# Kernel tuning notes

Measured on AMD Instinct MI355X. Metric: run time of the kernel, lower is better.

The kernel has to match this reference:

```python
import jax, jax.numpy as jnp
import numpy as np

B_, S_, E_ = 1, 2048, 2048
NH, P_, N_, G_, K_, CS = 64, 64, 128, 1, 4, 256
INTER = NH * P_            # 4096
CONV_DIM = INTER + 2 * G_ * N_  # 4352
PROJ = INTER + CONV_DIM + NH
EPS = 1e-5


def setup_inputs() -> dict:
    key = jax.random.key(0)
    ks = jax.random.split(key, 6)
    return {
        "input_states": jax.random.normal(ks[0], (B_, S_, E_), dtype=jnp.float32),
        "mask": jnp.ones((B_, 1, S_), dtype=jnp.int32),
        "W_in": jax.random.normal(ks[1], (PROJ, E_), dtype=jnp.float32) * 0.02,
        "conv_w": jax.random.normal(ks[2], (CONV_DIM, K_), dtype=jnp.float32) * 0.2,
        "conv_b": jnp.zeros((CONV_DIM,), dtype=jnp.float32),
        "dt_bias": jnp.ones((NH,), dtype=jnp.float32),
        "A_log": jnp.log(jnp.arange(1, NH + 1, dtype=jnp.float32)),
        "D": jnp.ones((NH,), dtype=jnp.float32),
        "norm_w": jnp.ones((INTER,), dtype=jnp.float32),
        "W_out": jax.random.normal(ks[3], (E_, INTER), dtype=jnp.float32) * 0.02,
    }


def segsum(x):
    # x: [..., L]; out[..., i, j] = sum_{j < k <= i} x[..., k], -inf above diagonal
    L = x.shape[-1]
    i = jnp.arange(L)
    strict = i[:, None] > i[None, :]
    X = jnp.where(strict, x[..., :, None], 0.0)   # [..., L(i), L(j)]
    S = jnp.cumsum(X, axis=-2)
    return jnp.where(i[:, None] >= i[None, :], S, -jnp.inf)


def reference(input_states, mask, W_in, conv_w, conv_b, dt_bias, A_log, D, norm_w, W_out):
    B, S, E = input_states.shape
    # mask has shape[1]==1 -> apply_mask_to_padding_states is a no-op
    proj = input_states @ W_in.T                      # [B,S,PROJ]
    gate = proj[..., :INTER]
    h_BC = proj[..., INTER:INTER + CONV_DIM]
    dt = proj[..., INTER + CONV_DIM:]                 # [B,S,NH]

    # causal depthwise conv1d (padding=K-1, truncated to seq_len)
    xpad = jnp.pad(h_BC, ((0, 0), (K_ - 1, 0), (0, 0)))
    conv = conv_b
    for i in range(K_):
        conv = conv + xpad[:, i:i + S, :] * conv_w[:, i]
    h_BC = jax.nn.silu(conv)

    hidden = h_BC[..., :INTER]
    Bm = h_BC[..., INTER:INTER + G_ * N_]
    Cm = h_BC[..., INTER + G_ * N_:]

    A = -jnp.exp(A_log)                               # [NH]
    dt = jnp.clip(jax.nn.softplus(dt + dt_bias), 0.0) # [B,S,NH]

    Hs = hidden.reshape(B, S, NH, P_).astype(jnp.float32)
    Bm = jnp.tile(Bm.reshape(B, S, G_, N_).astype(jnp.float32), (1, 1, NH // G_, 1))
    Cm = jnp.tile(Cm.reshape(B, S, G_, N_).astype(jnp.float32), (1, 1, NH // G_, 1))

    D_resid = D[None, None, :, None] * Hs             # pad=0 since S % CS == 0
    Hdt = Hs * dt[..., None]
    At = A * dt                                       # [B,S,NH]

    C_ = S // CS
    Hc = Hdt.reshape(B, C_, CS, NH, P_)
    Ac = At.reshape(B, C_, CS, NH)
    Bc = Bm.reshape(B, C_, CS, NH, N_)
    Cc = Cm.reshape(B, C_, CS, NH, N_)

    Ap = jnp.transpose(Ac, (0, 3, 1, 2))              # [B,H,C,L]
    A_cum = jnp.cumsum(Ap, axis=-1)                   # [B,H,C,L]
    L_tri = jnp.exp(segsum(Ap))                       # [B,H,C,L,L]

    # diagonal (intra-chunk) output
    Gm = jnp.einsum('bclhn,bcshn->bclsh', Cc, Bc)
    M = Gm * jnp.transpose(L_tri, (0, 2, 3, 4, 1))    # [B,C,L,S,H]
    Yd = jnp.einsum('bclsh,bcshp->bclhp', M, Hc)

    # per-chunk states (note: source uses same-chunk states, no inter-chunk scan)
    decay = jnp.exp(A_cum[..., -1:] - A_cum)          # [B,H,C,L]
    Bd = Bc * jnp.transpose(decay, (0, 2, 3, 1))[..., None]
    states = jnp.einsum('bclhn,bclhp->bchpn', Bd, Hc) # [B,C,H,P,N]

    Sd = jnp.transpose(jnp.exp(A_cum), (0, 2, 3, 1))  # [B,C,L,H]
    Yoff = jnp.einsum('bclhn,bchpn->bclhp', Cc, states) * Sd[..., None]

    y = (Yd + Yoff).reshape(B, S, NH, P_) + D_resid
    y = y.reshape(B, S, INTER)

    # gated RMSNorm (fp32)
    yf = y.astype(jnp.float32) * jax.nn.silu(gate.astype(jnp.float32))
    var = jnp.mean(yf * yf, axis=-1, keepdims=True)
    yn = norm_w * (yf * jax.lax.rsqrt(var + EPS))

    return yn @ W_out.T
```

## Files before the change

### kernel.cpp

```cpp
#include <hip/hip_runtime.h>
#include <math.h>

#define S_LEN   2048
#define E_DIM   2048
#define NH      64
#define P_DIM   64
#define N_DIM   128
#define CS      256
#define NCHUNK  8
#define INTER   4096
#define CONVD   4352
#define PROJ    8512
#define GEMM1N  8448
#define EPS     1e-5f

#define OFF_PROJBF 0ull
#define OFF_HBC    8650752ull
#define OFF_DTG    13107200ull
#define OFF_DTPART 13238272ull
#define OFF_GM     17432576ull
#define OFF_YV     17956864ull
#define OFF_R      26345472ull
#define OFF_WOUT   37093376ull

typedef __bf16 bf16x8 __attribute__((ext_vector_type(8)));
typedef float  f32x4  __attribute__((ext_vector_type(4)));
typedef float  f32x16 __attribute__((ext_vector_type(16)));

__device__ __forceinline__ float bf2f(unsigned short u) {
    union { unsigned int i; float f; } v; v.i = ((unsigned int)u) << 16; return v.f;
}
__device__ __forceinline__ unsigned short f2bf(float f) {
    union { float f; unsigned int i; } v; v.f = f;
    unsigned int r = v.i + 0x7FFFu + ((v.i >> 16) & 1u);
    return (unsigned short)(r >> 16);
}
__device__ __forceinline__ void gl_lds16(const void* g, void* l) {
    __builtin_amdgcn_global_load_lds(
        (const __attribute__((address_space(1))) void*)g,
        (__attribute__((address_space(3))) void*)l, 16, 0, 0);
}

__global__ __launch_bounds__(256) void cast3_kernel(
    const float* __restrict__ X, const float* __restrict__ Win,
    const float* __restrict__ Wout, unsigned short* __restrict__ Xbf,
    unsigned short* __restrict__ Winbf, unsigned short* __restrict__ Woutbf)
{
    const int blk = blockIdx.x;
    const float* src; unsigned short* dst; size_t off;
    if (blk < 2048)       { src = X;    dst = Xbf;    off = (size_t)blk * 2048; }
    else if (blk < 10496) { src = Win;  dst = Winbf;  off = (size_t)(blk - 2048) * 2048; }
    else                  { src = Wout; dst = Woutbf; off = (size_t)(blk - 10496) * 2048; }
    size_t i = off + (size_t)threadIdx.x * 8;
    float4 a = *(const float4*)(src + i);
    float4 b = *(const float4*)(src + i + 4);
    uint4 o;
    o.x = (unsigned int)f2bf(a.x) | ((unsigned int)f2bf(a.y) << 16);
    o.y = (unsigned int)f2bf(a.z) | ((unsigned int)f2bf(a.w) << 16);
    o.z = (unsigned int)f2bf(b.x) | ((unsigned int)f2bf(b.y) << 16);
    o.w = (unsigned int)f2bf(b.z) | ((unsigned int)f2bf(b.w) << 16);
    *(uint4*)(dst + i) = o;
}

#define WAITV(n) asm volatile("s_waitcnt vmcnt(" #n ")" ::: "memory")
#define BARR()   asm volatile("s_barrier" ::: "memory")

__global__ __launch_bounds__(512, 2) void gemm256_8ph(
    const unsigned short* __restrict__ A, int lda, long long sA,
    const unsigned short* __restrict__ B, int ldb, long long sB,
    float* __restrict__ Cf, unsigned short* __restrict__ Cb, int ldc,
    long long sC, int K, int mswap)
{
    __shared__ unsigned short sm[65536];
    A += (long long)blockIdx.z * sA;
    B += (long long)blockIdx.z * sB;
    const int t    = threadIdx.x;
    const int m0   = (mswap ? blockIdx.x : blockIdx.y) * 256;
    const int n0   = (mswap ? blockIdx.y : blockIdx.x) * 256;
    const int lane = t & 63;
    const int w    = t >> 6;
    const int wm   = ((w >> 2) & 1) * 64;
    const int wn   = (w & 3) * 32;
    const int l15  = lane & 15;
    const int l4   = lane >> 4;
    const int NT   = K >> 6;

    const int sr = t >> 3, sl = t & 7;

    auto STAGE = [&](int T, int h, int isB) {
        const unsigned short* G = isB ? B : A;
        const int ld   = isB ? ldb : lda;
        const int base = (isB ? n0 : m0) + h * 128;
        unsigned short* dst =
            &sm[(T & 1) * 32768 + isB * 16384 + h * 8192 + t * 8];
#pragma unroll
        for (int j = 0; j < 2; j++) {
            const int r   = sr + 64 * j;
            const int gch = sl ^ ((r ^ (r >> 3)) & 7);
            gl_lds16(G + (size_t)(base + r) * ld + T * 64 + gch * 8,
                     dst + j * 4096);
        }
    };

    int aoff[4], asw[4], boff[2], bsw[2];
#pragma unroll
    for (int mi = 0; mi < 4; mi++) {
        int r = wm + mi * 16 + l15;
        aoff[mi] = r * 64; asw[mi] = (r ^ (r >> 3)) & 7;
    }
#pragma unroll
    for (int ni = 0; ni < 2; ni++) {
        int r = wn + ni * 16 + l15;
        boff[ni] = r * 64; bsw[ni] = (r ^ (r >> 3)) & 7;
    }

    bf16x8 aF[4][2], bF[2][2][2];
    f32x4  acc[2][2][4][2];
#pragma unroll
    for (int qm = 0; qm < 2; qm++)
#pragma unroll
        for (int qn = 0; qn < 2; qn++)
#pragma unroll
            for (int mi = 0; mi < 4; mi++)
#pragma unroll
                for (int ni = 0; ni < 2; ni++)
                    acc[qm][qn][mi][ni] = (f32x4){0.f, 0.f, 0.f, 0.f};

#define LOAD_A(qm) do { \
    const unsigned short* p_ = &sm[cb + (qm) * 8192]; \
    _Pragma("unroll") for (int mi = 0; mi < 4; mi++) \
    _Pragma("unroll") for (int ks = 0; ks < 2; ks++) \
        aF[mi][ks] = *(const bf16x8*)&p_[aoff[mi] + \
            (((ks * 4 + l4) ^ asw[mi]) << 3)]; \
} while (0)
#define LOAD_B(qn) do { \
    const unsigned short* p_ = &sm[cb + 16384 + (qn) * 8192]; \
    _Pragma("unroll") for (int ni = 0; ni < 2; ni++) \
    _Pragma("unroll") for (int ks = 0; ks < 2; ks++) \
        bF[qn][ni][ks] = *(const bf16x8*)&p_[boff[ni] + \
            (((ks * 4 + l4) ^ bsw[ni]) << 3)]; \
} while (0)
#define MMA(qm, qn) do { \
    __builtin_amdgcn_s_setprio(1); \
    _Pragma("unroll") for (int ks = 0; ks < 2; ks++) \
    _Pragma("unroll") for (int mi = 0; mi < 4; mi++) \
    _Pragma("unroll") for (int ni = 0; ni < 2; ni++) \
        acc[qm][qn][mi][ni] = __builtin_amdgcn_mfma_f32_16x16x32_bf16( \
            aF[mi][ks], bF[qn][ni][ks], acc[qm][qn][mi][ni], 0, 0, 0); \
    __builtin_amdgcn_s_setprio(0); \
} while (0)

    STAGE(0, 0, 0);
    STAGE(0, 1, 1);
    STAGE(0, 0, 1);
    STAGE(0, 1, 0);
    STAGE(1, 0, 0);
    STAGE(1, 1, 1);
    WAITV(0);
    BARR();

    for (int tt = 0; tt < NT; tt++) {
        const int cb = (tt & 1) * 32768;
        if (tt + 1 < NT) { WAITV(6); } else { WAITV(2); }
        LOAD_A(0); LOAD_B(0);
        if (tt + 1 < NT) STAGE(tt + 1, 0, 1);
        BARR();
        MMA(0, 0);
        BARR();
        LOAD_B(1);
        if (tt + 1 < NT) STAGE(tt + 1, 1, 0);
        BARR();
        MMA(0, 1);
        BARR();
        if (tt + 1 < NT) { WAITV(6); } else { WAITV(0); }
        LOAD_A(1);
        if (tt + 2 < NT) STAGE(tt + 2, 0, 0);
        BARR();
        MMA(1, 1);
        BARR();
        if (tt + 2 < NT) STAGE(tt + 2, 1, 1);
        BARR();
        MMA(1, 0);
        BARR();
    }

#undef LOAD_A
#undef LOAD_B
#undef MMA

    if (Cb) {
#pragma unroll
        for (int qm = 0; qm < 2; qm++)
#pragma unroll
        for (int qn = 0; qn < 2; qn++)
#pragma unroll
        for (int mi = 0; mi < 4; mi++)
#pragma unroll
        for (int ni = 0; ni < 2; ni++) {
            const int rb = m0 + qm * 128 + wm + mi * 16 + l4 * 4;
            const int cc = n0 + qn * 128 + wn + ni * 16 + l15;
#pragma unroll
            for (int rr = 0; rr < 4; rr++)
                Cb[(size_t)(rb + rr) * ldc + cc] = f2bf(acc[qm][qn][mi][ni][rr]);
        }
    } else {
        float* Cz = Cf + (long long)blockIdx.z * sC;
#pragma unroll
        for (int qm = 0; qm < 2; qm++)
#pragma unroll
        for (int qn = 0; qn < 2; qn++)
#pragma unroll
        for (int mi = 0; mi < 4; mi++)
#pragma unroll
        for (int ni = 0; ni < 2; ni++) {
            const int rb = m0 + qm * 128 + wm + mi * 16 + l4 * 4;
            const int cc = n0 + qn * 128 + wn + ni * 16 + l15;
#pragma unroll
            for (int rr = 0; rr < 4; rr++)
                Cz[(size_t)(rb + rr) * ldc + cc] = acc[qm][qn][mi][ni][rr];
        }
    }
}

__global__ __launch_bounds__(256) void gemm_bt_mfma(
    const unsigned short* __restrict__ A, int lda, long long sA,
    const unsigned short* __restrict__ B, int ldb, long long sB,
    float* __restrict__ Cf, unsigned short* __restrict__ Cb, int ldc,
    long long sC, int K, int mswap)
{
    __shared__ unsigned short As[128 * 64];
    __shared__ unsigned short Bs[128 * 64];
    A += (long long)blockIdx.z * sA;
    B += (long long)blockIdx.z * sB;
    const int t     = threadIdx.x;
    const int m0    = (mswap ? blockIdx.x : blockIdx.y) * 128;
    const int n0    = (mswap ? blockIdx.y : blockIdx.x) * 128;
    const int w     = t >> 6;
    const int lane  = t & 63;
    const int col   = lane & 31;
    const int khalf = lane >> 5;
    const int wm    = (w & 1) * 64;
    const int wn    = (w >> 1) * 64;

    const int srow  = t >> 3;
    const int sslot = t & 7;
    const unsigned short* Agp[4];
    const unsigned short* Bgp[4];
#pragma unroll
    for (int i = 0; i < 4; i++) {
        const int r   = srow + 32 * i;
        const int gch = sslot ^ ((r ^ (r >> 3)) & 7);
        Agp[i] = A + (size_t)(m0 + r) * lda + gch * 8;
        Bgp[i] = B + (size_t)(n0 + r) * ldb + gch * 8;
    }
    unsigned short* Asl = &As[t * 8];
    unsigned short* Bsl = &Bs[t * 8];

    int aOff[2], aXor[2], bOff[2], bXor[2];
#pragma unroll
    for (int i = 0; i < 2; i++) {
        const int ra = wm + i * 32 + col;
        aOff[i] = ra * 64; aXor[i] = (ra ^ (ra >> 3)) & 7;
        const int rb = wn + i * 32 + col;
        bOff[i] = rb * 64; bXor[i] = (rb ^ (rb >> 3)) & 7;
    }

    f32x16 acc[2][2];
#pragma unroll
    for (int mi = 0; mi < 2; mi++)
#pragma unroll
        for (int ni = 0; ni < 2; ni++)
#pragma unroll
            for (int e = 0; e < 16; e++) acc[mi][ni][e] = 0.f;

    for (int k0 = 0; k0 < K; k0 += 64) {
        __syncthreads();
#pragma unroll
        for (int i = 0; i < 4; i++) {
            gl_lds16(Agp[i] + k0, Asl + i * 2048);
            gl_lds16(Bgp[i] + k0, Bsl + i * 2048);
        }
        __syncthreads();
#pragma unroll
        for (int ks = 0; ks < 4; ks++) {
            const int ch = ks * 2 + khalf;
            bf16x8 af[2], bfr[2];
#pragma unroll
            for (int i = 0; i < 2; i++) {
                af[i]  = *(const bf16x8*)&As[aOff[i] + ((ch ^ aXor[i]) * 8)];
                bfr[i] = *(const bf16x8*)&Bs[bOff[i] + ((ch ^ bXor[i]) * 8)];
            }
#pragma unroll
            for (int mi = 0; mi < 2; mi++)
#pragma unroll
                for (int ni = 0; ni < 2; ni++)
                    acc[mi][ni] = __builtin_amdgcn_mfma_f32_32x32x16_bf16(
                        af[mi], bfr[ni], acc[mi][ni], 0, 0, 0);
        }
    }

    if (Cb) {
#pragma unroll
        for (int mi = 0; mi < 2; mi++)
#pragma unroll
            for (int ni = 0; ni < 2; ni++) {
                const int rbase = m0 + wm + mi * 32 + 4 * khalf;
                const int cc    = n0 + wn + ni * 32 + col;
#pragma unroll
                for (int g = 0; g < 4; g++)
#pragma unroll
                    for (int rr = 0; rr < 4; rr++)
                        Cb[(size_t)(rbase + 8 * g + rr) * ldc + cc] =
                            f2bf(acc[mi][ni][4 * g + rr]);
            }
    } else {
        float* Cz = Cf + (long long)blockIdx.z * sC;
#pragma unroll
        for (int mi = 0; mi < 2; mi++)
#pragma unroll
            for (int ni = 0; ni < 2; ni++) {
                const int rbase = m0 + wm + mi * 32 + 4 * khalf;
                const int cc    = n0 + wn + ni * 32 + col;
#pragma unroll
                for (int g = 0; g < 4; g++)
#pragma unroll
                    for (int rr = 0; rr < 4; rr++)
                        Cz[(size_t)(rbase + 8 * g + rr) * ldc + cc] =
                            acc[mi][ni][4 * g + rr];
            }
    }
}

__global__ __launch_bounds__(256) void addf4_kernel(
    const float* __restrict__ p, float* __restrict__ o)
{
    size_t i = ((size_t)blockIdx.x * 256 + threadIdx.x) * 4;
    float4 a = *(const float4*)(p + i);
    float4 b = *(const float4*)(p + i + 4194304);
    float4 c = *(const float4*)(p + i + 8388608);
    float4 d = *(const float4*)(p + i + 12582912);
    float4 r = make_float4(a.x + b.x + c.x + d.x, a.y + b.y + c.y + d.y,
                           a.z + b.z + c.z + d.z, a.w + b.w + c.w + d.w);
    *(float4*)(o + i) = r;
}

__global__ __launch_bounds__(256) void gemm_nt(
    const float* __restrict__ A, int lda, long long sA,
    const float* __restrict__ B, int ldb, long long sB,
    float* __restrict__ C, int ldc, long long sC, int K)
{
    A += (long long)blockIdx.z * sA;
    B += (long long)blockIdx.z * sB;
    C += (long long)blockIdx.z * sC;
    const int t  = threadIdx.x;
    const int m0 = blockIdx.y * 128;
    const int n0 = blockIdx.x * 64;
    __shared__ float As[16][132];
    __shared__ float Bs[16][68];
    const int tx = t & 15;
    const int ty = t >> 4;

    const int arow = t & 127;
    const int akh  = (t >> 7) * 8;
    const float* Aload = A + (size_t)(m0 + arow) * (size_t)lda + akh;
    const int brow = t & 63;
    const int bk4  = (t >> 6) * 4;
    const float* Bload = B + (size_t)(n0 + brow) * (size_t)ldb + bk4;

    float acc[8][4];
#pragma unroll
    for (int i = 0; i < 8; i++)
#pragma unroll
        for (int j = 0; j < 4; j++) acc[i][j] = 0.f;

    for (int k0 = 0; k0 < K; k0 += 16) {
        __syncthreads();
        float4 a0 = *(const float4*)(Aload + k0);
        float4 a1 = *(const float4*)(Aload + k0 + 4);
        float4 b0 = *(const float4*)(Bload + k0);
        As[akh + 0][arow] = a0.x; As[akh + 1][arow] = a0.y;
        As[akh + 2][arow] = a0.z; As[akh + 3][arow] = a0.w;
        As[akh + 4][arow] = a1.x; As[akh + 5][arow] = a1.y;
        As[akh + 6][arow] = a1.z; As[akh + 7][arow] = a1.w;
        Bs[bk4 + 0][brow] = b0.x; Bs[bk4 + 1][brow] = b0.y;
        Bs[bk4 + 2][brow] = b0.z; Bs[bk4 + 3][brow] = b0.w;
        __syncthreads();
#pragma unroll
        for (int k = 0; k < 16; k++) {
            float4 a4 = *(const float4*)(&As[k][ty * 8]);
            float4 a5 = *(const float4*)(&As[k][ty * 8 + 4]);
            float4 b4 = *(const float4*)(&Bs[k][tx * 4]);
            float am[8] = {a4.x, a4.y, a4.z, a4.w, a5.x, a5.y, a5.z, a5.w};
            float bn[4] = {b4.x, b4.y, b4.z, b4.w};
#pragma unroll
            for (int i = 0; i < 8; i++)
#pragma unroll
                for (int j = 0; j < 4; j++) acc[i][j] += am[i] * bn[j];
        }
    }
#pragma unroll
    for (int i = 0; i < 8; i++) {
        float4 o = make_float4(acc[i][0], acc[i][1], acc[i][2], acc[i][3]);
        *(float4*)(C + (size_t)(m0 + ty * 8 + i) * (size_t)ldc + n0 + tx * 4) = o;
    }
}

__global__ __launch_bounds__(256) void dt_reduce_kernel(
    const float* __restrict__ part, const float* __restrict__ dt_bias,
    float* __restrict__ dtg)
{
    const int i = blockIdx.x * 256 + threadIdx.x;
    float x = dt_bias[i & 63];
#pragma unroll
    for (int z = 0; z < 32; z++) x += part[(size_t)z * 131072 + i];
    dtg[i] = (x > 20.f) ? x : log1pf(__expf(x));
}

__global__ __launch_bounds__(256) void conv_silu8_kernel(
    const unsigned short* __restrict__ projbf, const float* __restrict__ conv_w,
    const float* __restrict__ conv_b, unsigned short* __restrict__ out)
{
    const int c  = blockIdx.x * 256 + threadIdx.x;
    const int s0 = blockIdx.y * 8;
    const float4 w = *(const float4*)(conv_w + (size_t)c * 4);
    const float b = conv_b[c];
    const size_t base = 4096 + (size_t)c;
    float v[11];
#pragma unroll
    for (int m = 0; m < 11; m++) {
        int s = s0 - 3 + m;
        v[m] = (s >= 0) ? bf2f(projbf[(size_t)s * GEMM1N + base]) : 0.f;
    }
#pragma unroll
    for (int j = 0; j < 8; j++) {
        float acc = b + v[j] * w.x + v[j + 1] * w.y + v[j + 2] * w.z + v[j + 3] * w.w;
        float sig = 1.f / (1.f + __expf(-acc));
        out[(size_t)(s0 + j) * CONVD + c] = f2bf(acc * sig);
    }
}

__global__ __launch_bounds__(256, 2) void ssm_mfma_kernel(
    const unsigned short* __restrict__ hBC, const float* __restrict__ dtg,
    const float* __restrict__ Gm, const float* __restrict__ A_log,
    const float* __restrict__ Dp, float* __restrict__ y)
{
    const int h    = blockIdx.x;
    const int c    = blockIdx.y;
    const int t    = threadIdx.x;
    const int wid  = t >> 6;
    const int lane = t & 63;
    const int lo   = lane & 15;
    const int q    = lane >> 4;

    __shared__ float sAcum[CS], sdt[CS], sD[CS], sEs[CS], sDecay[CS], sScl[CS];
    __shared__ float sWaveSum[4];
    __shared__ unsigned short sHdtT[64 * 264];
    __shared__ unsigned short sStT[64 * 136];
    __shared__ unsigned short sBufB[128 * 72];

    const float A = -__expf(A_log[h]);
    const int row0 = c * CS;
    const unsigned short* hid = hBC + (size_t)row0 * CONVD + h * P_DIM;
    const unsigned short* Bp  = hBC + (size_t)row0 * CONVD + INTER;
    const unsigned short* Cp  = hBC + (size_t)row0 * CONVD + INTER + N_DIM;
    const float* gm = Gm + (size_t)c * CS * CS;

    float dtv = dtg[(size_t)(row0 + t) * NH + h];
    float v = A * dtv;
    for (int off = 1; off < 64; off <<= 1) {
        float u = __shfl_up(v, off, 64);
        if (lane >= off) v += u;
    }
    if (lane == 63) sWaveSum[wid] = v;
    __syncthreads();
    float pre = 0.f;
    for (int i = 0; i < 4; i++) if (i < wid) pre += sWaveSum[i];
    v += pre;
    sAcum[t] = v;
    sdt[t] = dtv;
    __syncthreads();
    const float AcumEnd = sAcum[CS - 1];
    {
        float ac   = sAcum[t];
        float apre = (t < 64) ? 0.f : sAcum[(t & ~63) - 1];
        sD[t]     = __expf(ac - apre);
        sEs[t]    = __expf(sAcum[t | 63] - ac);
        sDecay[t] = __expf(AcumEnd - ac);
        sScl[t]   = __expf(ac);
    }

    unsigned short* stgu = sStT;
    for (int lt = 0; lt < 4; lt++) {
        __syncthreads();
        {
            const int c8 = (t & 7) * 8;
#pragma unroll
            for (int j = 0; j < 2; j++) {
                int l = (t >> 3) + 32 * j;
                *(uint4*)&stgu[l * 64 + c8] =
                    *(const uint4*)(hid + (size_t)(lt * 64 + l) * CONVD + c8);
            }
        }
        __syncthreads();
        {
            const int p = t & 63, lq = (t >> 6) * 16;
#pragma unroll
            for (int j = 0; j < 4; j++) {
                ushort4 pk;
                int l0 = lq + j * 4;
                pk.x = f2bf(bf2f(stgu[(l0 + 0) * 64 + p]) * sdt[lt * 64 + l0 + 0]);
                pk.y = f2bf(bf2f(stgu[(l0 + 1) * 64 + p]) * sdt[lt * 64 + l0 + 1]);
                pk.z = f2bf(bf2f(stgu[(l0 + 2) * 64 + p]) * sdt[lt * 64 + l0 + 2]);
                pk.w = f2bf(bf2f(stgu[(l0 + 3) * 64 + p]) * sdt[lt * 64 + l0 + 3]);
                *(uint2*)&sHdtT[p * 264 + lt * 64 + l0] = *(uint2*)&pk;
            }
        }
    }

    f32x4 acc2[2][4];
#pragma unroll
    for (int mi = 0; mi < 2; mi++)
#pragma unroll
        for (int ni = 0; ni < 4; ni++) acc2[mi][ni] = (f32x4){0.f, 0.f, 0.f, 0.f};
    const int psub = (wid & 1) * 32;
    const int nsub = (wid >> 1) * 64;

    for (int qt = 0; qt < 4; qt++) {
        for (int hf = 0; hf < 2; hf++) {
            __syncthreads();
            {
                const int n8 = (t & 15) * 8;
#pragma unroll
                for (int j = 0; j < 2; j++) {
                    int r = (t >> 4) + 16 * j;
                    *(uint4*)&stgu[r * 128 + n8] =
                        *(const uint4*)(Bp + (size_t)(qt * 64 + hf * 32 + r) * CONVD + n8);
                }
            }
            __syncthreads();
            {
                const int n = t & 127, lc = (t >> 7) * 16;
#pragma unroll
                for (int j = 0; j < 4; j++) {
                    int l0 = lc + j * 4;
                    ushort4 pk;
                    pk.x = f2bf(bf2f(stgu[(l0 + 0) * 128 + n]) * sDecay[qt * 64 + hf * 32 + l0 + 0]);
                    pk.y = f2bf(bf2f(stgu[(l0 + 1) * 128 + n]) * sDecay[qt * 64 + hf * 32 + l0 + 1]);
                    pk.z = f2bf(bf2f(stgu[(l0 + 2) * 128 + n]) * sDecay[qt * 64 + hf * 32 + l0 + 2]);
                    pk.w = f2bf(bf2f(stgu[(l0 + 3) * 128 + n]) * sDecay[qt * 64 + hf * 32 + l0 + 3]);
                    *(uint2*)&sBufB[n * 72 + hf * 32 + l0] = *(uint2*)&pk;
                }
            }
        }
        __syncthreads();
#pragma unroll
        for (int ks = 0; ks < 2; ks++) {
            const int k0 = qt * 64 + ks * 32;
            const int kq = ks * 32;
            bf16x8 a2[2], b2[4];
#pragma unroll
            for (int mi = 0; mi < 2; mi++)
                a2[mi] = *(const bf16x8*)&sHdtT[(psub + mi * 16 + lo) * 264 + k0 + q * 8];
#pragma unroll
            for (int ni = 0; ni < 4; ni++)
                b2[ni] = *(const bf16x8*)&sBufB[(nsub + ni * 16 + lo) * 72 + kq + q * 8];
#pragma unroll
            for (int mi = 0; mi < 2; mi++)
#pragma unroll
                for (int ni = 0; ni < 4; ni++)
                    acc2[mi][ni] = __builtin_amdgcn_mfma_f32_16x16x32_bf16(
                        a2[mi], b2[ni], acc2[mi][ni], 0, 0, 0);
        }
    }
    __syncthreads();
#pragma unroll
    for (int mi = 0; mi < 2; mi++)
#pragma unroll
        for (int ni = 0; ni < 4; ni++)
#pragma unroll
            for (int rr = 0; rr < 4; rr++) {
                int p = psub + mi * 16 + q * 4 + rr;
                int n = nsub + ni * 16 + lo;
                sStT[p * 136 + n] = f2bf(acc2[mi][ni][rr]);
            }

    f32x4 accY[4][2][2];
#pragma unroll
    for (int i = 0; i < 4; i++)
#pragma unroll
        for (int mi = 0; mi < 2; mi++)
#pragma unroll
            for (int pi = 0; pi < 2; pi++) accY[i][mi][pi] = (f32x4){0.f, 0.f, 0.f, 0.f};
    const int pcol = (wid & 1) * 32;
    const int rsub = (wid >> 1) * 16;
    unsigned short* Cs = sBufB;

    for (int i = 0; i < 4; i++) {
        __syncthreads();
        {
            const int n8 = (t & 15) * 8;
#pragma unroll
            for (int j = 0; j < 4; j++) {
                int r = (t >> 4) + 16 * j;
                uint4 cv = *(const uint4*)(Cp + (size_t)(i * 64 + r) * CONVD + n8);
                float scl = sScl[i * 64 + r];
                const unsigned short* cu = (const unsigned short*)&cv;
                ushort4 p0, p1;
                p0.x = f2bf(bf2f(cu[0]) * scl); p0.y = f2bf(bf2f(cu[1]) * scl);
                p0.z = f2bf(bf2f(cu[2]) * scl); p0.w = f2bf(bf2f(cu[3]) * scl);
                p1.x = f2bf(bf2f(cu[4]) * scl); p1.y = f2bf(bf2f(cu[5]) * scl);
                p1.z = f2bf(bf2f(cu[6]) * scl); p1.w = f2bf(bf2f(cu[7]) * scl);
                *(uint2*)&Cs[r * 136 + n8]     = *(uint2*)&p0;
                *(uint2*)&Cs[r * 136 + n8 + 4] = *(uint2*)&p1;
            }
        }
        __syncthreads();
#pragma unroll
        for (int ks = 0; ks < 4; ks++) {
            const int k0 = ks * 32;
            bf16x8 a3[2], b3[2];
#pragma unroll
            for (int mi = 0; mi < 2; mi++)
                a3[mi] = *(const bf16x8*)&Cs[(mi * 32 + rsub + lo) * 136 + k0 + q * 8];
#pragma unroll
            for (int pi = 0; pi < 2; pi++)
                b3[pi] = *(const bf16x8*)&sStT[(pcol + pi * 16 + lo) * 136 + k0 + q * 8];
#pragma unroll
            for (int mi = 0; mi < 2; mi++)
#pragma unroll
                for (int pi = 0; pi < 2; pi++)
                    accY[i][mi][pi] = __builtin_amdgcn_mfma_f32_16x16x32_bf16(
                        a3[mi], b3[pi], accY[i][mi][pi], 0, 0, 0);
        }
    }

    unsigned short* Mt = sBufB;
    for (int i = 0; i < 4; i++) {
        const int nk = 2 * (i + 1);
        for (int mi = 0; mi < 2; mi++) {
            __syncthreads();
            if (wid <= i) {
                float P = 1.f;
                for (int m = wid + 1; m <= i - 1; m++) P *= sD[m * 64 + 63];
                const int s4 = wid * 64 + lo * 4;
                float4 es4 = *(const float4*)&sEs[s4];
#pragma unroll
                for (int j = 0; j < 8; j++) {
                    int lr = q + j * 4;
                    int l  = i * 64 + mi * 32 + lr;
                    float4 g4 = *(const float4*)&gm[(size_t)l * CS + s4];
                    float w0, w1, w2, w3;
                    if (wid == i) {
                        float al = sAcum[l];
                        w0 = (s4 + 0 <= l) ? __expf(al - sAcum[s4 + 0]) : 0.f;
                        w1 = (s4 + 1 <= l) ? __expf(al - sAcum[s4 + 1]) : 0.f;
                        w2 = (s4 + 2 <= l) ? __expf(al - sAcum[s4 + 2]) : 0.f;
                        w3 = (s4 + 3 <= l) ? __expf(al - sAcum[s4 + 3]) : 0.f;
                    } else {
                        float rs = sD[l] * P;
                        w0 = rs * es4.x; w1 = rs * es4.y;
                        w2 = rs * es4.z; w3 = rs * es4.w;
                    }
                    ushort4 pk;
                    pk.x = f2bf(g4.x * w0); pk.y = f2bf(g4.y * w1);
                    pk.z = f2bf(g4.z * w2); pk.w = f2bf(g4.w * w3);
                    *(uint2*)&Mt[lr * 264 + s4] = *(uint2*)&pk;
                }
            }
            __syncthreads();
            for (int ks = 0; ks < nk; ks++) {
                const int k0 = ks * 32;
                bf16x8 am = *(const bf16x8*)&Mt[(rsub + lo) * 264 + k0 + q * 8];
                bf16x8 b1[2];
#pragma unroll
                for (int pi = 0; pi < 2; pi++)
                    b1[pi] = *(const bf16x8*)&sHdtT[(pcol + pi * 16 + lo) * 264 + k0 + q * 8];
#pragma unroll
                for (int pi = 0; pi < 2; pi++)
                    accY[i][mi][pi] = __builtin_amdgcn_mfma_f32_16x16x32_bf16(
                        am, b1[pi], accY[i][mi][pi], 0, 0, 0);
            }
        }
    }

    const float Dh = Dp[h];
#pragma unroll
    for (int i = 0; i < 4; i++)
#pragma unroll
        for (int mi = 0; mi < 2; mi++)
#pragma unroll
            for (int pi = 0; pi < 2; pi++)
#pragma unroll
                for (int rr = 0; rr < 4; rr++) {
                    int l = i * 64 + mi * 32 + rsub + q * 4 + rr;
                    int p = pcol + pi * 16 + lo;
                    float hv = bf2f(hid[(size_t)l * CONVD + p]);
                    y[(size_t)(row0 + l) * INTER + h * P_DIM + p] =
                        accY[i][mi][pi][rr] + Dh * hv;
                }
}

__global__ __launch_bounds__(256) void norm_kernel(
    const float* __restrict__ y, const unsigned short* __restrict__ projbf,
    const float* __restrict__ norm_w, unsigned short* __restrict__ yn)
{
    const int s = blockIdx.x;
    const int t = threadIdx.x;
    __shared__ float sYf[INTER];
    __shared__ float sW[4];
    const float* yrow = y + (size_t)s * INTER;
    const unsigned short* grow = projbf + (size_t)s * GEMM1N;
    float sum = 0.f;
    for (int j0 = 0; j0 < INTER; j0 += 2048) {
        int j = j0 + t * 8;
        float4 y0 = *(const float4*)(yrow + j);
        float4 y1 = *(const float4*)(yrow + j + 4);
        uint4 gp = *(const uint4*)(grow + j);
        float gv[8] = {
            bf2f((unsigned short)(gp.x & 0xffff)), bf2f((unsigned short)(gp.x >> 16)),
            bf2f((unsigned short)(gp.y & 0xffff)), bf2f((unsigned short)(gp.y >> 16)),
            bf2f((unsigned short)(gp.z & 0xffff)), bf2f((unsigned short)(gp.z >> 16)),
            bf2f((unsigned short)(gp.w & 0xffff)), bf2f((unsigned short)(gp.w >> 16))};
        float yv8[8] = {y0.x, y0.y, y0.z, y0.w, y1.x, y1.y, y1.z, y1.w};
#pragma unroll
        for (int e = 0; e < 8; e++) {
            float f = yv8[e] * (gv[e] / (1.f + __expf(-gv[e])));
            sum += f * f;
            sYf[j + e] = f;
        }
    }
    for (int off = 32; off > 0; off >>= 1) sum += __shfl_down(sum, off, 64);
    if ((t & 63) == 0) sW[t >> 6] = sum;
    __syncthreads();
    const float var = (sW[0] + sW[1] + sW[2] + sW[3]) * (1.f / (float)INTER);
    const float rs = rsqrtf(var + EPS);
    for (int j0 = 0; j0 < INTER; j0 += 2048) {
        int j = j0 + t * 8;
        float4 w0 = *(const float4*)(norm_w + j);
        float4 w1 = *(const float4*)(norm_w + j + 4);
        float wv[8] = {w0.x, w0.y, w0.z, w0.w, w1.x, w1.y, w1.z, w1.w};
        unsigned short o[8];
#pragma unroll
        for (int e = 0; e < 8; e++) o[e] = f2bf(sYf[j + e] * wv[e] * rs);
        uint4 ov;
        ov.x = (unsigned int)o[0] | ((unsigned int)o[1] << 16);
        ov.y = (unsigned int)o[2] | ((unsigned int)o[3] << 16);
        ov.z = (unsigned int)o[4] | ((unsigned int)o[5] << 16);
        ov.w = (unsigned int)o[6] | ((unsigned int)o[7] << 16);
        *(uint4*)(yn + (size_t)s * INTER + j) = ov;
    }
}

extern "C" void kernel_launch(void* const* d_in, const int* in_sizes, int n_in,
                              void* d_out, int out_size, void* d_ws, size_t ws_size,
                              hipStream_t stream)
{
    const float* X       = (const float*)d_in[0];
    const float* W_in    = (const float*)d_in[2];
    const float* conv_w  = (const float*)d_in[3];
    const float* conv_b  = (const float*)d_in[4];
    const float* dt_bias = (const float*)d_in[5];
    const float* A_log   = (const float*)d_in[6];
    const float* Dp      = (const float*)d_in[7];
    const float* norm_w  = (const float*)d_in[8];
    const float* W_out   = (const float*)d_in[9];
    float* out = (float*)d_out;
    float* ws  = (float*)d_ws;

    unsigned short* projbf = (unsigned short*)(ws + OFF_PROJBF);
    unsigned short* hbc16  = (unsigned short*)(ws + OFF_HBC);
    float* dtg     = ws + OFF_DTG;
    float* dtpart  = ws + OFF_DTPART;
    float* gm      = ws + OFF_GM;
    float* yv      = ws + OFF_YV;
    unsigned short* Xbf    = (unsigned short*)(ws + OFF_R);
    unsigned short* Winbf  = (unsigned short*)(ws + OFF_R + 2097152);
    unsigned short* ynbf   = (unsigned short*)(ws + OFF_R);
    unsigned short* Woutbf = (unsigned short*)(ws + OFF_WOUT);
    float* part = ws;

    cast3_kernel<<<14592, 256, 0, stream>>>(X, W_in, W_out, Xbf, Winbf, Woutbf);

    gemm_bt_mfma<<<dim3(S_LEN / 128, GEMM1N / 128, 1), 256, 0, stream>>>(
        Xbf, E_DIM, 0LL, Winbf, E_DIM, 0LL, nullptr, projbf, GEMM1N, 0LL,
        E_DIM, 1);

    gemm_nt<<<dim3(1, 16, 32), 256, 0, stream>>>(
        X, E_DIM, 64LL, W_in + (size_t)GEMM1N * E_DIM, E_DIM, 64LL,
        dtpart, NH, 131072LL, 64);
    dt_reduce_kernel<<<512, 256, 0, stream>>>(dtpart, dt_bias, dtg);

    conv_silu8_kernel<<<dim3(CONVD / 256, S_LEN / 8), 256, 0, stream>>>(
        projbf, conv_w, conv_b, hbc16);

    gemm_bt_mfma<<<dim3(CS / 128, CS / 128, NCHUNK), 256, 0, stream>>>(
        hbc16 + INTER + N_DIM, CONVD, (long long)CS * CONVD,
        hbc16 + INTER,         CONVD, (long long)CS * CONVD,
        gm, nullptr, CS, (long long)CS * CS, N_DIM, 0);

    ssm_mfma_kernel<<<dim3(NH, NCHUNK), 256, 0, stream>>>(
        hbc16, dtg, gm, A_log, Dp, yv);

    norm_kernel<<<dim3(S_LEN), 256, 0, stream>>>(yv, projbf, norm_w, ynbf);

    gemm256_8ph<<<dim3(E_DIM / 256, S_LEN / 256, 4), 512, 0, stream>>>(
        ynbf, INTER, 1024LL, Woutbf, INTER, 1024LL,
        part, nullptr, E_DIM, 4194304LL, 1024, 0);
    addf4_kernel<<<4096, 256, 0, stream>>>(part, out);
}
```

Measured before the change: 410.1 us.

## Route input projection through 256x256 tile GEMM with fused N-tail computation

The big input projection GEMM (2048x8448x2048) moves from the 128x128-tile kernel to the 512-thread 256x256 8-phase kernel. That kernel covers the first 8192 columns. The remaining 256 tail columns are computed by an extra per-block epilogue: each of the 256 blocks does a 16x128 slice with direct-from-global MFMA loads and register double-buffering. The intent is higher MFMA efficiency and reuse from the larger tiles on the dominant GEMM. The cost is a serialized tail phase in every block that reads uncached operands from global memory.

```diff
diff --git a/kernel.cpp b/kernel.cpp
--- a/kernel.cpp
+++ b/kernel.cpp
@@ -69,7 +69,7 @@
     const unsigned short* __restrict__ A, int lda, long long sA,
     const unsigned short* __restrict__ B, int ldb, long long sB,
     float* __restrict__ Cf, unsigned short* __restrict__ Cb, int ldc,
-    long long sC, int K, int mswap)
+    long long sC, int K, int mswap, int tailN)
 {
     __shared__ unsigned short sm[65536];
     A += (long long)blockIdx.z * sA;
@@ -220,6 +220,43 @@
                 Cz[(size_t)(rb + rr) * ldc + cc] = acc[qm][qn][mi][ni][rr];
         }
     }
+
+    if (tailN && Cb) {
+        const int bid  = mswap ? (blockIdx.y * gridDim.x + blockIdx.x)
+                               : (blockIdx.x * gridDim.y + blockIdx.y);
+        const int mr0  = (bid >> 1) * 16;
+        const int nc0  = tailN + (bid & 1) * 128;
+        const int wnt  = w * 16;
+        const unsigned short* ap = A + (size_t)(mr0 + l15) * lda + l4 * 8;
+        const unsigned short* bp = B + (size_t)(nc0 + wnt + l15) * ldb + l4 * 8;
+        f32x4 tacc = (f32x4){0.f, 0.f, 0.f, 0.f};
+        bf16x8 ta[4], tb[4], na[4], nb[4];
+#pragma unroll
+        for (int u = 0; u < 4; u++) {
+            ta[u] = *(const bf16x8*)(ap + u * 32);
+            tb[u] = *(const bf16x8*)(bp + u * 32);
+            na[u] = ta[u]; nb[u] = tb[u];
+        }
+        for (int kt = 0; kt < K; kt += 128) {
+            if (kt + 128 < K) {
+#pragma unroll
+                for (int u = 0; u < 4; u++) {
+                    na[u] = *(const bf16x8*)(ap + kt + 128 + u * 32);
+                    nb[u] = *(const bf16x8*)(bp + kt + 128 + u * 32);
+                }
+            }
+#pragma unroll
+            for (int u = 0; u < 4; u++)
+                tacc = __builtin_amdgcn_mfma_f32_16x16x32_bf16(
+                    ta[u], tb[u], tacc, 0, 0, 0);
+#pragma unroll
+            for (int u = 0; u < 4; u++) { ta[u] = na[u]; tb[u] = nb[u]; }
+        }
+#pragma unroll
+        for (int rr = 0; rr < 4; rr++)
+            Cb[(size_t)(mr0 + l4 * 4 + rr) * ldc + nc0 + wnt + l15] =
+                f2bf(tacc[rr]);
+    }
 }
 
 __global__ __launch_bounds__(256) void gemm_bt_mfma(
@@ -781,9 +818,9 @@
 
     cast3_kernel<<<14592, 256, 0, stream>>>(X, W_in, W_out, Xbf, Winbf, Woutbf);
 
-    gemm_bt_mfma<<<dim3(S_LEN / 128, GEMM1N / 128, 1), 256, 0, stream>>>(
+    gemm256_8ph<<<dim3(S_LEN / 256, 8192 / 256, 1), 512, 0, stream>>>(
         Xbf, E_DIM, 0LL, Winbf, E_DIM, 0LL, nullptr, projbf, GEMM1N, 0LL,
-        E_DIM, 1);
+        E_DIM, 1, 8192);
 
     gemm_nt<<<dim3(1, 16, 32), 256, 0, stream>>>(
         X, E_DIM, 64LL, W_in + (size_t)GEMM1N * E_DIM, E_DIM, 64LL,
@@ -805,6 +842,6 @@
 
     gemm256_8ph<<<dim3(E_DIM / 256, S_LEN / 256, 4), 512, 0, stream>>>(
         ynbf, INTER, 1024LL, Woutbf, INTER, 1024LL,
-        part, nullptr, E_DIM, 4194304LL, 1024, 0);
+        part, nullptr, E_DIM, 4194304LL, 1024, 0, 0);
     addf4_kernel<<<4096, 256, 0, stream>>>(part, out);
 }
```

After: 425.6 us. 1.04x slower.

## Move vmcnt waits after MMAs and add occupancy-bounded projection GEMM kernel

Applied to the files above, without the earlier changes.

The 256x256 GEMM loop now waits on outstanding global loads at the end of each MMA phase rather than before the LDS reads, so memory latency overlaps with the math. The projection GEMM is moved to a new kernel variant that wraps the shared 128-tile body with launch_bounds(256,4) and drops the batched-stride arguments, which pushes register use down to allow more resident blocks. The bf16 output path of the large-tile kernel gains a per-z offset. Risks are spills from the tighter register budget and subtle wait-count mistakes in the reordered pipeline.

```diff
diff --git a/kernel.cpp b/kernel.cpp
--- a/kernel.cpp
+++ b/kernel.cpp
@@ -161,7 +161,6 @@
 
     for (int tt = 0; tt < NT; tt++) {
         const int cb = (tt & 1) * 32768;
-        if (tt + 1 < NT) { WAITV(6); } else { WAITV(2); }
         LOAD_A(0); LOAD_B(0);
         if (tt + 1 < NT) STAGE(tt + 1, 0, 1);
         BARR();
@@ -171,8 +170,8 @@
         if (tt + 1 < NT) STAGE(tt + 1, 1, 0);
         BARR();
         MMA(0, 1);
+        if (tt + 1 < NT) { WAITV(8); } else { WAITV(0); }
         BARR();
-        if (tt + 1 < NT) { WAITV(6); } else { WAITV(0); }
         LOAD_A(1);
         if (tt + 2 < NT) STAGE(tt + 2, 0, 0);
         BARR();
@@ -181,6 +180,8 @@
         if (tt + 2 < NT) STAGE(tt + 2, 1, 1);
         BARR();
         MMA(1, 0);
+        if (tt + 2 < NT)      { WAITV(6); }
+        else if (tt + 1 < NT) { WAITV(2); }
         BARR();
     }
 
@@ -189,6 +190,7 @@
 #undef MMA
 
     if (Cb) {
+        unsigned short* Cz = Cb + (long long)blockIdx.z * sC;
 #pragma unroll
         for (int qm = 0; qm < 2; qm++)
 #pragma unroll
@@ -201,7 +203,7 @@
             const int cc = n0 + qn * 128 + wn + ni * 16 + l15;
 #pragma unroll
             for (int rr = 0; rr < 4; rr++)
-                Cb[(size_t)(rb + rr) * ldc + cc] = f2bf(acc[qm][qn][mi][ni][rr]);
+                Cz[(size_t)(rb + rr) * ldc + cc] = f2bf(acc[qm][qn][mi][ni][rr]);
         }
     } else {
         float* Cz = Cf + (long long)blockIdx.z * sC;
@@ -222,19 +224,14 @@
     }
 }
 
-__global__ __launch_bounds__(256) void gemm_bt_mfma(
-    const unsigned short* __restrict__ A, int lda, long long sA,
-    const unsigned short* __restrict__ B, int ldb, long long sB,
+__device__ __forceinline__ void gemm_bt_body(
+    const unsigned short* __restrict__ A, int lda,
+    const unsigned short* __restrict__ B, int ldb,
     float* __restrict__ Cf, unsigned short* __restrict__ Cb, int ldc,
-    long long sC, int K, int mswap)
-{
-    __shared__ unsigned short As[128 * 64];
-    __shared__ unsigned short Bs[128 * 64];
-    A += (long long)blockIdx.z * sA;
-    B += (long long)blockIdx.z * sB;
+    int K, int m0, int n0,
+    unsigned short* As, unsigned short* Bs)
+{
     const int t     = threadIdx.x;
-    const int m0    = (mswap ? blockIdx.x : blockIdx.y) * 128;
-    const int n0    = (mswap ? blockIdx.y : blockIdx.x) * 128;
     const int w     = t >> 6;
     const int lane  = t & 63;
     const int col   = lane & 31;
@@ -314,7 +311,6 @@
                             f2bf(acc[mi][ni][4 * g + rr]);
             }
     } else {
-        float* Cz = Cf + (long long)blockIdx.z * sC;
 #pragma unroll
         for (int mi = 0; mi < 2; mi++)
 #pragma unroll
@@ -325,10 +321,38 @@
                 for (int g = 0; g < 4; g++)
 #pragma unroll
                     for (int rr = 0; rr < 4; rr++)
-                        Cz[(size_t)(rbase + 8 * g + rr) * ldc + cc] =
+                        Cf[(size_t)(rbase + 8 * g + rr) * ldc + cc] =
                             acc[mi][ni][4 * g + rr];
             }
     }
+}
+
+__global__ __launch_bounds__(256) void gemm_bt_mfma(
+    const unsigned short* __restrict__ A, int lda, long long sA,
+    const unsigned short* __restrict__ B, int ldb, long long sB,
+    float* __restrict__ Cf, unsigned short* __restrict__ Cb, int ldc,
+    long long sC, int K, int mswap)
+{
+    __shared__ unsigned short As[128 * 64];
+    __shared__ unsigned short Bs[128 * 64];
+    A += (long long)blockIdx.z * sA;
+    B += (long long)blockIdx.z * sB;
+    float* Cz = Cf ? Cf + (long long)blockIdx.z * sC : nullptr;
+    const int m0 = (mswap ? blockIdx.x : blockIdx.y) * 128;
+    const int n0 = (mswap ? blockIdx.y : blockIdx.x) * 128;
+    gemm_bt_body(A, lda, B, ldb, Cz, Cb, ldc, K, m0, n0, As, Bs);
+}
+
+__global__ __launch_bounds__(256, 4) void gemm_bt_mfma4(
+    const unsigned short* __restrict__ A, int lda,
+    const unsigned short* __restrict__ B, int ldb,
+    unsigned short* __restrict__ Cb, int ldc, int K, int mswap)
+{
+    __shared__ unsigned short As[128 * 64];
+    __shared__ unsigned short Bs[128 * 64];
+    const int m0 = (mswap ? blockIdx.x : blockIdx.y) * 128;
+    const int n0 = (mswap ? blockIdx.y : blockIdx.x) * 128;
+    gemm_bt_body(A, lda, B, ldb, nullptr, Cb, ldc, K, m0, n0, As, Bs);
 }
 
 __global__ __launch_bounds__(256) void addf4_kernel(
@@ -781,9 +805,8 @@
 
     cast3_kernel<<<14592, 256, 0, stream>>>(X, W_in, W_out, Xbf, Winbf, Woutbf);
 
-    gemm_bt_mfma<<<dim3(S_LEN / 128, GEMM1N / 128, 1), 256, 0, stream>>>(
-        Xbf, E_DIM, 0LL, Winbf, E_DIM, 0LL, nullptr, projbf, GEMM1N, 0LL,
-        E_DIM, 1);
+    gemm_bt_mfma4<<<dim3(S_LEN / 128, GEMM1N / 128, 1), 256, 0, stream>>>(
+        Xbf, E_DIM, Winbf, E_DIM, projbf, GEMM1N, E_DIM, 1);
 
     gemm_nt<<<dim3(1, 16, 32), 256, 0, stream>>>(
         X, E_DIM, 64LL, W_in + (size_t)GEMM1N * E_DIM, E_DIM, 64LL,
```

Result: no change. 414.9 us (+1.2%).
